# Performance work log

Hardware: AMD Instinct MI355X
Metric: run time of the kernel (lower is better)

The kernel has to match this reference:

```python
import jax, jax.numpy as jnp
import numpy as np

N_NODES = 50000
NEG_SLOPE = 0.2


def gat_layer(x, src, dst, W, a_src, a_dst, b, concat):
    # x: [N, Fin]; W: [Fin, H*C]; a_src/a_dst: [H, C]; b: [H*C] or [C]
    H, C = a_src.shape
    h = (x @ W).reshape(-1, H, C)                      # [N, H, C]
    al_s = jnp.einsum('nhc,hc->nh', h, a_src)          # [N, H]
    al_d = jnp.einsum('nhc,hc->nh', h, a_dst)          # [N, H]
    e = jax.nn.leaky_relu(al_s[src] + al_d[dst], NEG_SLOPE)   # [E, H]
    # segment softmax over incoming edges of each destination node
    e_max = jax.ops.segment_max(e, dst, num_segments=N_NODES)  # [N, H]
    ex = jnp.exp(e - e_max[dst])
    denom = jax.ops.segment_sum(ex, dst, num_segments=N_NODES)
    alpha = ex / (denom[dst] + 1e-16)                  # [E, H]
    msg = h[src] * alpha[:, :, None]                   # [E, H, C]
    out = jax.ops.segment_sum(msg, dst, num_segments=N_NODES)  # [N, H, C]
    out = out.reshape(N_NODES, H * C) if concat else out.mean(axis=1)
    return out + b


def setup_inputs() -> dict:
    key = jax.random.key(0)
    ks = jax.random.split(key, 16)
    x = jax.random.normal(ks[0], (N_NODES, 12), dtype=jnp.float32)
    edge_index = jax.random.randint(ks[1], (2, 400000), 0, N_NODES, dtype=jnp.int32)
    H, C = 8, 64
    s = 0.1
    W1 = jax.random.normal(ks[2], (12, H * C), jnp.float32) * s
    as1 = jax.random.normal(ks[3], (H, C), jnp.float32) * s
    ad1 = jax.random.normal(ks[4], (H, C), jnp.float32) * s
    b1 = jnp.zeros((H * C,), jnp.float32)
    W2 = jax.random.normal(ks[5], (H * C, H * C), jnp.float32) * s
    as2 = jax.random.normal(ks[6], (H, C), jnp.float32) * s
    ad2 = jax.random.normal(ks[7], (H, C), jnp.float32) * s
    b2 = jnp.zeros((H * C,), jnp.float32)
    W3 = jax.random.normal(ks[8], (H * C, H * 5), jnp.float32) * s
    as3 = jax.random.normal(ks[9], (H, 5), jnp.float32) * s
    ad3 = jax.random.normal(ks[10], (H, 5), jnp.float32) * s
    b3 = jnp.zeros((5,), jnp.float32)
    return {"x": x, "edge_index": edge_index,
            "W1": W1, "as1": as1, "ad1": ad1, "b1": b1,
            "W2": W2, "as2": as2, "ad2": ad2, "b2": b2,
            "W3": W3, "as3": as3, "ad3": ad3, "b3": b3}


def reference(x, edge_index, W1, as1, ad1, b1, W2, as2, ad2, b2, W3, as3, ad3, b3):
    # add self-loops (PyG GATConv default add_self_loops=True)
    loop = jnp.arange(N_NODES, dtype=edge_index.dtype)
    src = jnp.concatenate([edge_index[0], loop])
    dst = jnp.concatenate([edge_index[1], loop])
    h = gat_layer(x, src, dst, W1, as1, ad1, b1, concat=True)
    h = jax.nn.relu(h)
    h = gat_layer(h, src, dst, W2, as2, ad2, b2, concat=True)
    h = jax.nn.relu(h)
    h = gat_layer(h, src, dst, W3, as3, ad3, b3, concat=False)
    return jax.nn.log_softmax(h, axis=1)
```

## Files before the change

### kernel.cpp

```cpp
#include <hip/hip_runtime.h>
#include <hip/hip_bf16.h>

#define NN    50000
#define MP    50048
#define E0C   400000
#define ETOT  450000
#define HH    8
#define FF    512
#define F3    40
#define C3    5
#define MAXE  128
#define NBLK  ((NN + 1023) / 1024)
#define MT2   (MP / 128)
#define GT2   (MT2 * 4)

typedef __attribute__((ext_vector_type(8))) short bf16x8;
typedef __attribute__((ext_vector_type(8))) short s16x8;
typedef __attribute__((ext_vector_type(4))) float f32x4;

__device__ inline unsigned short f2bf(float f) {
    union { float f; unsigned int u; } v; v.f = f;
    unsigned int r = v.u + 0x7FFF + ((v.u >> 16) & 1);
    return (unsigned short)(r >> 16);
}
__device__ inline float bf2f(unsigned short u) {
    union { unsigned int i; float f; } v; v.i = ((unsigned int)u) << 16;
    return v.f;
}

__global__ void count_kernel(const int* __restrict__ ei, int* __restrict__ cnt) {
    int e = blockIdx.x * blockDim.x + threadIdx.x;
    if (e >= ETOT) return;
    int dst = (e < E0C) ? ei[E0C + e] : (e - E0C);
    atomicAdd(&cnt[dst], 1);
}

__global__ __launch_bounds__(1024) void scan_blocks(const int* __restrict__ cnt,
                                                    int* __restrict__ offs,
                                                    int* __restrict__ bsum) {
    __shared__ int s[1024];
    int tid = threadIdx.x;
    int i = blockIdx.x * 1024 + tid;
    s[tid] = (i < NN) ? cnt[i] : 0;
    __syncthreads();
    for (int d = 1; d < 1024; d <<= 1) {
        int add = (tid >= d) ? s[tid - d] : 0;
        __syncthreads();
        s[tid] += add;
        __syncthreads();
    }
    if (i < NN) offs[i + 1] = s[tid];
    if (tid == 1023) bsum[blockIdx.x] = s[1023];
}

__global__ __launch_bounds__(64) void scan_sums(int* __restrict__ bsum) {
    int lane = threadIdx.x;
    int v = (lane < NBLK) ? bsum[lane] : 0;
    int orig = v;
#pragma unroll
    for (int d = 1; d < 64; d <<= 1) {
        int o = __shfl_up(v, d);
        if (lane >= d) v += o;
    }
    if (lane < NBLK) bsum[lane] = v - orig;
}

__global__ __launch_bounds__(1024) void scan_add(int* __restrict__ offs,
                                                 const int* __restrict__ bsum) {
    int i = blockIdx.x * 1024 + threadIdx.x;
    if (i < NN) offs[i + 1] += bsum[blockIdx.x];
    if (i == 0) offs[0] = 0;
}

__global__ void scatter_kernel(const int* __restrict__ ei, const int* __restrict__ offs,
                               int* __restrict__ cur, int* __restrict__ srcs) {
    int e = blockIdx.x * blockDim.x + threadIdx.x;
    if (e >= ETOT) return;
    int src, dst;
    if (e < E0C) { src = ei[e]; dst = ei[E0C + e]; }
    else         { src = dst = e - E0C; }
    int pos = offs[dst] + atomicAdd(&cur[dst], 1);
    srcs[pos] = src;
}

__global__ __launch_bounds__(256) void gemm1_fused(
    const float* __restrict__ x, const float* __restrict__ W1,
    const float* __restrict__ as1, const float* __restrict__ ad1,
    unsigned short* __restrict__ hb, float* __restrict__ al_s,
    float* __restrict__ al_d) {
    __shared__ float xs[64 * 12];
    int t = threadIdx.x;
    int n0 = blockIdx.x * 64;
    int nvalid = NN - n0; if (nvalid > 64) nvalid = 64;

    for (int j = t; j < nvalid * 12; j += 256) xs[j] = x[(size_t)n0 * 12 + j];
    __syncthreads();

    int f = t * 2;
    float w0[12], w1[12];
#pragma unroll
    for (int k = 0; k < 12; ++k) {
        float2 wv = *(const float2*)&W1[k * FF + f];
        w0[k] = wv.x; w1[k] = wv.y;
    }
    float2 asv = *(const float2*)&as1[f];
    float2 adv = *(const float2*)&ad1[f];
    int head = t >> 5;

    for (int ni = 0; ni < nvalid; ++ni) {
        const float* xp = &xs[ni * 12];
        float4 xa = *(const float4*)xp;
        float4 xb = *(const float4*)(xp + 4);
        float4 xc = *(const float4*)(xp + 8);
        float xv[12] = {xa.x, xa.y, xa.z, xa.w, xb.x, xb.y, xb.z, xb.w,
                        xc.x, xc.y, xc.z, xc.w};
        float h0 = 0.f, h1 = 0.f;
#pragma unroll
        for (int k = 0; k < 12; ++k) { h0 += xv[k] * w0[k]; h1 += xv[k] * w1[k]; }
        unsigned int u = ((unsigned int)f2bf(h1) << 16) | f2bf(h0);
        *(unsigned int*)&hb[(size_t)(n0 + ni) * FF + f] = u;
        float ps = h0 * asv.x + h1 * asv.y;
        float pd = h0 * adv.x + h1 * adv.y;
#pragma unroll
        for (int d = 1; d < 32; d <<= 1) {
            ps += __shfl_xor(ps, d);
            pd += __shfl_xor(pd, d);
        }
        if ((t & 31) == 0) {
            al_s[(size_t)(n0 + ni) * HH + head] = ps;
            al_d[(size_t)(n0 + ni) * HH + head] = pd;
        }
    }
}

__global__ __launch_bounds__(256) void attn_gather(
    const unsigned short* __restrict__ Hb,
    const float* __restrict__ alS, const float* __restrict__ alD,
    const int* __restrict__ offs, const int* __restrict__ srcs,
    const float* __restrict__ bias,
    float* __restrict__ out_f32, unsigned short* __restrict__ out_b16, int relu) {
    __shared__ float alpha_sh[4][MAXE][HH];
    __shared__ int   srcs_sh[4][MAXE];
    int w = threadIdx.x >> 6, lane = threadIdx.x & 63;
    int n = blockIdx.x * 4 + w;
    if (n >= NN) return;
    int h = lane >> 3, es = lane & 7;
    int beg = offs[n], end = offs[n + 1], deg = end - beg;

    float ald = alD[n * HH + h];
    float m = -1e30f, den = 0.f, idn;

    if (deg <= MAXE) {
        for (int e = es; e < deg; e += 8) {
            int s = srcs[beg + e];
            if (h == 0) srcs_sh[w][e] = s;
            float sc = alS[s * HH + h] + ald;
            sc = sc > 0.f ? sc : 0.2f * sc;
            alpha_sh[w][e][h] = sc;
            m = fmaxf(m, sc);
        }
        m = fmaxf(m, __shfl_xor(m, 1));
        m = fmaxf(m, __shfl_xor(m, 2));
        m = fmaxf(m, __shfl_xor(m, 4));
        for (int e = es; e < deg; e += 8) {
            float ex = __expf(alpha_sh[w][e][h] - m);
            den += ex;
            alpha_sh[w][e][h] = ex;
        }
        den += __shfl_xor(den, 1);
        den += __shfl_xor(den, 2);
        den += __shfl_xor(den, 4);
        idn = 1.f / (den + 1e-16f);
    } else {
        for (int e = es; e < deg; e += 8) {
            int s = srcs[beg + e];
            float sc = alS[s * HH + h] + ald;
            sc = sc > 0.f ? sc : 0.2f * sc;
            m = fmaxf(m, sc);
        }
        m = fmaxf(m, __shfl_xor(m, 1));
        m = fmaxf(m, __shfl_xor(m, 2));
        m = fmaxf(m, __shfl_xor(m, 4));
        for (int e = es; e < deg; e += 8) {
            int s = srcs[beg + e];
            float sc = alS[s * HH + h] + ald;
            sc = sc > 0.f ? sc : 0.2f * sc;
            den += __expf(sc - m);
        }
        den += __shfl_xor(den, 1);
        den += __shfl_xor(den, 2);
        den += __shfl_xor(den, 4);
        idn = 1.f / (den + 1e-16f);
    }

    int f0 = lane * 8;
    float acc[8] = {};
    if (deg <= MAXE) {
        int e = 0;
        for (; e + 4 <= deg; e += 4) {
            int s0 = srcs_sh[w][e + 0], s1 = srcs_sh[w][e + 1];
            int s2 = srcs_sh[w][e + 2], s3 = srcs_sh[w][e + 3];
            bf16x8 v0 = *(const bf16x8*)&Hb[(size_t)s0 * FF + f0];
            bf16x8 v1 = *(const bf16x8*)&Hb[(size_t)s1 * FF + f0];
            bf16x8 v2 = *(const bf16x8*)&Hb[(size_t)s2 * FF + f0];
            bf16x8 v3 = *(const bf16x8*)&Hb[(size_t)s3 * FF + f0];
            float a0 = alpha_sh[w][e + 0][h], a1 = alpha_sh[w][e + 1][h];
            float a2 = alpha_sh[w][e + 2][h], a3 = alpha_sh[w][e + 3][h];
#pragma unroll
            for (int k = 0; k < 8; ++k) {
                acc[k] += a0 * bf2f((unsigned short)v0[k]);
                acc[k] += a1 * bf2f((unsigned short)v1[k]);
                acc[k] += a2 * bf2f((unsigned short)v2[k]);
                acc[k] += a3 * bf2f((unsigned short)v3[k]);
            }
        }
        for (; e < deg; ++e) {
            int s = srcs_sh[w][e];
            float a = alpha_sh[w][e][h];
            bf16x8 v = *(const bf16x8*)&Hb[(size_t)s * FF + f0];
#pragma unroll
            for (int k = 0; k < 8; ++k)
                acc[k] += a * bf2f((unsigned short)v[k]);
        }
#pragma unroll
        for (int k = 0; k < 8; ++k) acc[k] *= idn;
    } else {
        for (int e = 0; e < deg; ++e) {
            int s = srcs[beg + e];
            float sc = alS[s * HH + h] + ald;
            sc = sc > 0.f ? sc : 0.2f * sc;
            float a = __expf(sc - m) * idn;
            bf16x8 v = *(const bf16x8*)&Hb[(size_t)s * FF + f0];
#pragma unroll
            for (int k = 0; k < 8; ++k)
                acc[k] += a * bf2f((unsigned short)v[k]);
        }
    }
    float4 b0 = *(const float4*)&bias[f0];
    float4 b1 = *(const float4*)&bias[f0 + 4];
    float bv[8] = {b0.x, b0.y, b0.z, b0.w, b1.x, b1.y, b1.z, b1.w};
    float vv[8];
#pragma unroll
    for (int k = 0; k < 8; ++k) {
        float t = acc[k] + bv[k];
        vv[k] = relu ? fmaxf(t, 0.f) : t;
    }
    if (out_f32) {
        float4 o0 = {vv[0], vv[1], vv[2], vv[3]};
        float4 o1 = {vv[4], vv[5], vv[6], vv[7]};
        *(float4*)&out_f32[(size_t)n * FF + f0] = o0;
        *(float4*)&out_f32[(size_t)n * FF + f0 + 4] = o1;
    }
    if (out_b16) {
        s16x8 ov;
#pragma unroll
        for (int k = 0; k < 8; ++k) ov[k] = (short)f2bf(vv[k]);
        *(s16x8*)&out_b16[(size_t)n * FF + f0] = ov;
    }
}

__global__ void prep_w2t(const float* __restrict__ W2, unsigned short* __restrict__ W2T) {
    int i = blockIdx.x * blockDim.x + threadIdx.x;
    if (i >= FF * FF) return;
    int n = i >> 9, k = i & 511;
    W2T[i] = f2bf(W2[k * FF + n]);
}

__global__ void prep_w3t(const float* __restrict__ W3, unsigned short* __restrict__ W3T) {
    int i = blockIdx.x * blockDim.x + threadIdx.x;
    if (i >= 48 * 512) return;
    int n = i >> 9, k = i & 511;
    W3T[i] = (n < F3) ? f2bf(W3[k * F3 + n]) : 0;
}

__global__ __launch_bounds__(256) void gemm_mfma(
    const unsigned short* __restrict__ A,
    const unsigned short* __restrict__ BT,
    const float* __restrict__ a_s, const float* __restrict__ a_d,
    unsigned short* __restrict__ Cb,
    float* __restrict__ alS, float* __restrict__ alD,
    int N, int K) {
    __shared__ unsigned short As[2][128 * 64];
    __shared__ unsigned short Bs[2][128 * 64];
    int t = threadIdx.x;
    int wave = t >> 6, lane = t & 63;
    int wr = wave >> 1, wc = wave & 1;

    int bid = blockIdx.x;
    int mt, nt;
    if (bid < (MT2 / 8) * 32) {
        int g = bid >> 5, r = bid & 31;
        mt = g * 8 + (r & 7);
        nt = r >> 3;
    } else {
        int t2 = bid - (MT2 / 8) * 32;
        mt = (MT2 / 8) * 8 + (t2 >> 2);
        nt = t2 & 3;
    }
    int m0 = mt * 128, n0 = nt * 128;

    f32x4 acc[4][4] = {};
    int kg = lane >> 4;
    int lr = lane & 15;

    auto STAGE = [&](int buf, int k0) {
#pragma unroll
        for (int q = 0; q < 4; ++q) {
            int c   = q * 256 + t;
            int row = c >> 3, kc = c & 7;
            int kcs = kc ^ (row & 7);
            const unsigned short* ga = A + (size_t)(m0 + row) * K + k0 + kcs * 8;
            const unsigned short* gb = BT + (size_t)(n0 + row) * K + k0 + kcs * 8;
            unsigned short* la = &As[buf][(size_t)(q * 256 + wave * 64) * 8];
            unsigned short* lb = &Bs[buf][(size_t)(q * 256 + wave * 64) * 8];
            __builtin_amdgcn_global_load_lds(
                (const __attribute__((address_space(1))) void*)ga,
                (__attribute__((address_space(3))) void*)la, 16, 0, 0);
            __builtin_amdgcn_global_load_lds(
                (const __attribute__((address_space(1))) void*)gb,
                (__attribute__((address_space(3))) void*)lb, 16, 0, 0);
        }
    };

    const int NT = K / 64;
    STAGE(0, 0);
    __syncthreads();
    int cur = 0;
    for (int kt = 0; kt < NT; ++kt) {
        if (kt + 1 < NT) STAGE(cur ^ 1, (kt + 1) * 64);
        const unsigned short* Ac = As[cur];
        const unsigned short* Bc = Bs[cur];
#pragma unroll
        for (int ks = 0; ks < 2; ++ks) {
            bf16x8 af[4], bf[4];
#pragma unroll
            for (int i = 0; i < 4; ++i) {
                int rowa = wr * 64 + i * 16 + lr;
                af[i] = *(const bf16x8*)&Ac[rowa * 64 + (((ks << 2) | kg) ^ (rowa & 7)) * 8];
                int rowb = wc * 64 + i * 16 + lr;
                bf[i] = *(const bf16x8*)&Bc[rowb * 64 + (((ks << 2) | kg) ^ (rowb & 7)) * 8];
            }
#pragma unroll
            for (int i = 0; i < 4; ++i)
#pragma unroll
                for (int j = 0; j < 4; ++j)
                    acc[i][j] = __builtin_amdgcn_mfma_f32_16x16x32_bf16(
                        af[i], bf[j], acc[i][j], 0, 0, 0);
        }
        __syncthreads();
        cur ^= 1;
    }

    int head = (n0 >> 6) + wc;
    float asv[4], adv[4];
#pragma unroll
    for (int j = 0; j < 4; ++j) {
        int cc = n0 + wc * 64 + j * 16 + lr;
        asv[j] = a_s[cc];
        adv[j] = a_d[cc];
    }
#pragma unroll
    for (int i = 0; i < 4; ++i) {
#pragma unroll
        for (int reg = 0; reg < 4; ++reg) {
            float ps = 0.f, pd = 0.f;
#pragma unroll
            for (int j = 0; j < 4; ++j) {
                ps += acc[i][j][reg] * asv[j];
                pd += acc[i][j][reg] * adv[j];
            }
#pragma unroll
            for (int d = 1; d < 16; d <<= 1) {
                ps += __shfl_xor(ps, d);
                pd += __shfl_xor(pd, d);
            }
            if (lr == 0) {
                int r = m0 + wr * 64 + i * 16 + kg * 4 + reg;
                alS[(size_t)r * HH + head] = ps;
                alD[(size_t)r * HH + head] = pd;
            }
        }
    }

#pragma unroll
    for (int i = 0; i < 4; ++i) {
        int rb = m0 + wr * 64 + i * 16 + kg * 4;
#pragma unroll
        for (int j = 0; j < 4; ++j) {
            int cc = n0 + wc * 64 + j * 16 + lr;
#pragma unroll
            for (int reg = 0; reg < 4; ++reg)
                Cb[(size_t)(rb + reg) * N + cc] = f2bf(acc[i][j][reg]);
        }
    }
}

__global__ __launch_bounds__(256) void gemm3_mfma(
    const unsigned short* __restrict__ A,
    const unsigned short* __restrict__ BT,
    float* __restrict__ C) {
    __shared__ unsigned short As[128 * 64];
    __shared__ unsigned short Bs[48 * 64];
    int t = threadIdx.x;
    int wave = t >> 6, lane = t & 63;
    int m0 = blockIdx.x * 128;
    int kg = lane >> 4, lr = lane & 15;

    f32x4 acc[2][3] = {};

    for (int k0 = 0; k0 < 512; k0 += 64) {
#pragma unroll
        for (int q = 0; q < 4; ++q) {
            int c   = q * 256 + t;
            int row = c >> 3, kc = c & 7;
            int kcs = kc ^ (row & 7);
            const unsigned short* ga = A + (size_t)(m0 + row) * 512 + k0 + kcs * 8;
            unsigned short* la = &As[(size_t)(q * 256 + wave * 64) * 8];
            __builtin_amdgcn_global_load_lds(
                (const __attribute__((address_space(1))) void*)ga,
                (__attribute__((address_space(3))) void*)la, 16, 0, 0);
        }
        {
            int c   = t;
            int row = c >> 3, kc = c & 7;
            int kcs = kc ^ (row & 7);
            const unsigned short* gb = BT + (size_t)row * 512 + k0 + kcs * 8;
            unsigned short* lb = &Bs[(size_t)(wave * 64) * 8];
            __builtin_amdgcn_global_load_lds(
                (const __attribute__((address_space(1))) void*)gb,
                (__attribute__((address_space(3))) void*)lb, 16, 0, 0);
        }
        if (t < 128) {
            int c   = 256 + t;
            int row = c >> 3, kc = c & 7;
            int kcs = kc ^ (row & 7);
            const unsigned short* gb = BT + (size_t)row * 512 + k0 + kcs * 8;
            unsigned short* lb = &Bs[(size_t)(256 + wave * 64) * 8];
            __builtin_amdgcn_global_load_lds(
                (const __attribute__((address_space(1))) void*)gb,
                (__attribute__((address_space(3))) void*)lb, 16, 0, 0);
        }
        __syncthreads();
#pragma unroll
        for (int ks = 0; ks < 2; ++ks) {
            bf16x8 af[2], bf[3];
#pragma unroll
            for (int i = 0; i < 2; ++i) {
                int rowa = wave * 32 + i * 16 + lr;
                af[i] = *(const bf16x8*)&As[rowa * 64 + (((ks << 2) | kg) ^ (rowa & 7)) * 8];
            }
#pragma unroll
            for (int j = 0; j < 3; ++j) {
                int rowb = j * 16 + lr;
                bf[j] = *(const bf16x8*)&Bs[rowb * 64 + (((ks << 2) | kg) ^ (rowb & 7)) * 8];
            }
#pragma unroll
            for (int i = 0; i < 2; ++i)
#pragma unroll
                for (int j = 0; j < 3; ++j)
                    acc[i][j] = __builtin_amdgcn_mfma_f32_16x16x32_bf16(
                        af[i], bf[j], acc[i][j], 0, 0, 0);
        }
        __syncthreads();
    }

#pragma unroll
    for (int i = 0; i < 2; ++i) {
        int rb = m0 + wave * 32 + i * 16 + kg * 4;
#pragma unroll
        for (int j = 0; j < 3; ++j) {
            int cc = j * 16 + lr;
            if (cc >= F3) continue;
#pragma unroll
            for (int reg = 0; reg < 4; ++reg) {
                int r = rb + reg;
                if (r < NN) C[(size_t)r * F3 + cc] = acc[i][j][reg];
            }
        }
    }
}

__global__ void al40_kernel(const float* __restrict__ h3, const float* __restrict__ as3,
                            const float* __restrict__ ad3, float* __restrict__ al_s,
                            float* __restrict__ al_d) {
    int n = blockIdx.x * blockDim.x + threadIdx.x;
    if (n >= NN) return;
#pragma unroll
    for (int hh = 0; hh < HH; ++hh) {
        float s = 0.f, d = 0.f;
#pragma unroll
        for (int c = 0; c < C3; ++c) {
            float v = h3[(size_t)n * F3 + hh * C3 + c];
            s += v * as3[hh * C3 + c];
            d += v * ad3[hh * C3 + c];
        }
        al_s[n * HH + hh] = s;
        al_d[n * HH + hh] = d;
    }
}

__global__ __launch_bounds__(256) void attn3_kernel(
    const float* __restrict__ h3, const float* __restrict__ al_s,
    const float* __restrict__ al_d, const int* __restrict__ offs,
    const int* __restrict__ srcs, const float* __restrict__ b3,
    float* __restrict__ out) {
    __shared__ float alpha_sh[4][MAXE][HH];
    __shared__ int   srcs_sh[4][MAXE];
    __shared__ float idn_sh[4][HH], m_sh[4][HH], ald_sh2[4][HH];
    __shared__ float accs[4][F3];
    __shared__ float vv[4][C3];
    int w = threadIdx.x >> 6, lane = threadIdx.x & 63;
    int n = blockIdx.x * 4 + w;
    int h = lane >> 3, es = lane & 7;
    int beg = offs[n], end = offs[n + 1], deg = end - beg;

    float ald = al_d[n * HH + h];
    float m = -1e30f, den = 0.f, idn;
    if (deg <= MAXE) {
        for (int e = es; e < deg; e += 8) {
            int s = srcs[beg + e];
            if (h == 0) srcs_sh[w][e] = s;
            float sc = al_s[s * HH + h] + ald;
            sc = sc > 0.f ? sc : 0.2f * sc;
            alpha_sh[w][e][h] = sc;
            m = fmaxf(m, sc);
        }
        m = fmaxf(m, __shfl_xor(m, 1));
        m = fmaxf(m, __shfl_xor(m, 2));
        m = fmaxf(m, __shfl_xor(m, 4));
        for (int e = es; e < deg; e += 8) {
            float ex = __expf(alpha_sh[w][e][h] - m);
            den += ex;
            alpha_sh[w][e][h] = ex;
        }
        den += __shfl_xor(den, 1);
        den += __shfl_xor(den, 2);
        den += __shfl_xor(den, 4);
        idn = 1.f / (den + 1e-16f);
        if (es == 0) idn_sh[w][h] = idn;
    } else {
        for (int e = es; e < deg; e += 8) {
            int s = srcs[beg + e];
            float sc = al_s[s * HH + h] + ald;
            sc = sc > 0.f ? sc : 0.2f * sc;
            m = fmaxf(m, sc);
        }
        m = fmaxf(m, __shfl_xor(m, 1));
        m = fmaxf(m, __shfl_xor(m, 2));
        m = fmaxf(m, __shfl_xor(m, 4));
        for (int e = es; e < deg; e += 8) {
            int s = srcs[beg + e];
            float sc = al_s[s * HH + h] + ald;
            sc = sc > 0.f ? sc : 0.2f * sc;
            den += __expf(sc - m);
        }
        den += __shfl_xor(den, 1);
        den += __shfl_xor(den, 2);
        den += __shfl_xor(den, 4);
        idn = 1.f / (den + 1e-16f);
        if (es == 0) { idn_sh[w][h] = idn; m_sh[w][h] = m; ald_sh2[w][h] = ald; }
    }
    __syncthreads();

    if (lane < F3) {
        int hh = lane / C3;
        float acc = 0.f;
        if (deg <= MAXE) {
            int e = 0;
            for (; e + 4 <= deg; e += 4) {
                int s0 = srcs_sh[w][e + 0], s1 = srcs_sh[w][e + 1];
                int s2 = srcs_sh[w][e + 2], s3 = srcs_sh[w][e + 3];
                float v0 = h3[(size_t)s0 * F3 + lane];
                float v1 = h3[(size_t)s1 * F3 + lane];
                float v2 = h3[(size_t)s2 * F3 + lane];
                float v3 = h3[(size_t)s3 * F3 + lane];
                acc += alpha_sh[w][e + 0][hh] * v0 + alpha_sh[w][e + 1][hh] * v1
                     + alpha_sh[w][e + 2][hh] * v2 + alpha_sh[w][e + 3][hh] * v3;
            }
            for (; e < deg; ++e) {
                int s = srcs_sh[w][e];
                acc += alpha_sh[w][e][hh] * h3[(size_t)s * F3 + lane];
            }
        } else {
            float mm = m_sh[w][hh], aald = ald_sh2[w][hh];
            for (int e = 0; e < deg; ++e) {
                int s = srcs[beg + e];
                float sc = al_s[s * HH + hh] + aald;
                sc = sc > 0.f ? sc : 0.2f * sc;
                acc += __expf(sc - mm) * h3[(size_t)s * F3 + lane];
            }
        }
        accs[w][lane] = acc * idn_sh[w][hh];
    }
    __syncthreads();
    if (lane < C3) {
        float s = 0.f;
#pragma unroll
        for (int hh = 0; hh < HH; ++hh) s += accs[w][hh * C3 + lane];
        vv[w][lane] = s * 0.125f + b3[lane];
    }
    __syncthreads();
    if (lane < C3) {
        float mx = vv[w][0];
#pragma unroll
        for (int c = 1; c < C3; ++c) mx = fmaxf(mx, vv[w][c]);
        float se = 0.f;
#pragma unroll
        for (int c = 0; c < C3; ++c) se += __expf(vv[w][c] - mx);
        out[(size_t)n * C3 + lane] = vv[w][lane] - mx - logf(se);
    }
}

extern "C" void kernel_launch(void* const* d_in, const int* in_sizes, int n_in,
                              void* d_out, int out_size, void* d_ws, size_t ws_size,
                              hipStream_t stream) {
    const float* x   = (const float*)d_in[0];
    const int*   ei  = (const int*)d_in[1];
    const float* W1  = (const float*)d_in[2];
    const float* as1 = (const float*)d_in[3];
    const float* ad1 = (const float*)d_in[4];
    const float* b1  = (const float*)d_in[5];
    const float* W2  = (const float*)d_in[6];
    const float* as2 = (const float*)d_in[7];
    const float* ad2 = (const float*)d_in[8];
    const float* b2  = (const float*)d_in[9];
    const float* W3  = (const float*)d_in[10];
    const float* as3 = (const float*)d_in[11];
    const float* ad3 = (const float*)d_in[12];
    const float* b3  = (const float*)d_in[13];
    float* out = (float*)d_out;

    auto au = [](size_t v) { return (v + 255) & ~(size_t)255; };
    char* p = (char*)d_ws;
    size_t szHb = au((size_t)MP * FF * 2);
    char* r1 = p;
    unsigned short* Hb1 = (unsigned short*)r1;
    unsigned short* Hb2 = (unsigned short*)r1;
    p += szHb;
    char* r2 = p;
    unsigned short* A2   = (unsigned short*)r2;
    unsigned short* Bb16 = (unsigned short*)r2;
    unsigned short* W2T  = (unsigned short*)(r2 + szHb);
    p = r2 + szHb + au((size_t)FF * FF * 2);
    unsigned short* W3T = (unsigned short*)p;  p += au((size_t)48 * 512 * 2);
    float* alS  = (float*)p;  p += au((size_t)MP * HH * 4);
    float* alD  = (float*)p;  p += au((size_t)MP * HH * 4);
    float* h3   = (float*)p;  p += au((size_t)NN * F3 * 4);
    int* offs   = (int*)p;    p += au((size_t)(NN + 1) * 4);
    int* cnt    = (int*)p;    p += au((size_t)NN * 4);
    int* srcs   = (int*)p;    p += au((size_t)ETOT * 4);
    int* bsum   = (int*)p;    p += au(64 * 4);

    hipMemsetAsync(cnt, 0, (size_t)NN * 4, stream);
    count_kernel<<<(ETOT + 255) / 256, 256, 0, stream>>>(ei, cnt);
    scan_blocks<<<NBLK, 1024, 0, stream>>>(cnt, offs, bsum);
    scan_sums<<<1, 64, 0, stream>>>(bsum);
    scan_add<<<NBLK, 1024, 0, stream>>>(offs, bsum);
    hipMemsetAsync(cnt, 0, (size_t)NN * 4, stream);
    scatter_kernel<<<(ETOT + 255) / 256, 256, 0, stream>>>(ei, offs, cnt, srcs);
    hipMemsetAsync(A2 + (size_t)NN * FF, 0, (size_t)(MP - NN) * FF * 2, stream);
    prep_w2t<<<(FF * FF + 255) / 256, 256, 0, stream>>>(W2, W2T);
    prep_w3t<<<(48 * 512 + 255) / 256, 256, 0, stream>>>(W3, W3T);

    gemm1_fused<<<(NN + 63) / 64, 256, 0, stream>>>(x, W1, as1, ad1, Hb1, alS, alD);
    attn_gather<<<(NN + 3) / 4, 256, 0, stream>>>(Hb1, alS, alD, offs, srcs, b1,
                                                  nullptr, A2, 1);

    gemm_mfma<<<GT2, 256, 0, stream>>>(
        A2, W2T, as2, ad2, Hb2, alS, alD, FF, FF);
    attn_gather<<<(NN + 3) / 4, 256, 0, stream>>>(Hb2, alS, alD, offs, srcs, b2,
                                                  nullptr, Bb16, 1);

    gemm3_mfma<<<MP / 128, 256, 0, stream>>>(Bb16, W3T, h3);
    al40_kernel<<<(NN + 255) / 256, 256, 0, stream>>>(h3, as3, ad3, alS, alD);
    attn3_kernel<<<NN / 4, 256, 0, stream>>>(h3, alS, alD, offs, srcs, b3, out);
}
```

Before: 351.6 us.

## Fuse scan and prep launches; single-buffer LDS in layer-2 GEMM

Folds the block-sum scan into scan_add, so each block computes its own prefix with a wave reduction. Merges the W2/W3 transpose-convert kernels and the A2 padding memset into one prep kernel. Together these drop three launches from the pipeline. It also switches the layer-2 MFMA GEMM from double-buffered to single-buffered LDS, with a sync after each stage. That halves shared memory and may raise occupancy, but global loads no longer overlap with MFMA compute.

```diff
diff --git a/kernel.cpp b/kernel.cpp
--- a/kernel.cpp
+++ b/kernel.cpp
@@ -53,22 +53,19 @@
     if (tid == 1023) bsum[blockIdx.x] = s[1023];
 }
 
-__global__ __launch_bounds__(64) void scan_sums(int* __restrict__ bsum) {
-    int lane = threadIdx.x;
-    int v = (lane < NBLK) ? bsum[lane] : 0;
-    int orig = v;
-#pragma unroll
-    for (int d = 1; d < 64; d <<= 1) {
-        int o = __shfl_up(v, d);
-        if (lane >= d) v += o;
-    }
-    if (lane < NBLK) bsum[lane] = v - orig;
-}
-
 __global__ __launch_bounds__(1024) void scan_add(int* __restrict__ offs,
                                                  const int* __restrict__ bsum) {
-    int i = blockIdx.x * 1024 + threadIdx.x;
-    if (i < NN) offs[i + 1] += bsum[blockIdx.x];
+    __shared__ int pref;
+    int tid = threadIdx.x;
+    if (tid < 64) {
+        int v = (tid < blockIdx.x) ? bsum[tid] : 0;
+#pragma unroll
+        for (int d = 32; d; d >>= 1) v += __shfl_xor(v, d);
+        if (tid == 0) pref = v;
+    }
+    __syncthreads();
+    int i = blockIdx.x * 1024 + tid;
+    if (i < NN) offs[i + 1] += pref;
     if (i == 0) offs[0] = 0;
 }
 
@@ -81,6 +78,25 @@
     else         { src = dst = e - E0C; }
     int pos = offs[dst] + atomicAdd(&cur[dst], 1);
     srcs[pos] = src;
+}
+
+__global__ void prep_all(const float* __restrict__ W2, const float* __restrict__ W3,
+                         unsigned short* __restrict__ W2T, unsigned short* __restrict__ W3T,
+                         unsigned short* __restrict__ A2) {
+    int i = blockIdx.x * blockDim.x + threadIdx.x;
+    if (i < FF * FF) {
+        int n = i >> 9, k = i & 511;
+        W2T[i] = f2bf(W2[k * FF + n]);
+        return;
+    }
+    int j = i - FF * FF;
+    if (j < 48 * 512) {
+        int n = j >> 9, k = j & 511;
+        W3T[j] = (n < F3) ? f2bf(W3[k * F3 + n]) : 0;
+        return;
+    }
+    int l = j - 48 * 512;
+    if (l < (MP - NN) * FF) A2[(size_t)NN * FF + l] = 0;
 }
 
 __global__ __launch_bounds__(256) void gemm1_fused(
@@ -259,20 +275,6 @@
     }
 }
 
-__global__ void prep_w2t(const float* __restrict__ W2, unsigned short* __restrict__ W2T) {
-    int i = blockIdx.x * blockDim.x + threadIdx.x;
-    if (i >= FF * FF) return;
-    int n = i >> 9, k = i & 511;
-    W2T[i] = f2bf(W2[k * FF + n]);
-}
-
-__global__ void prep_w3t(const float* __restrict__ W3, unsigned short* __restrict__ W3T) {
-    int i = blockIdx.x * blockDim.x + threadIdx.x;
-    if (i >= 48 * 512) return;
-    int n = i >> 9, k = i & 511;
-    W3T[i] = (n < F3) ? f2bf(W3[k * F3 + n]) : 0;
-}
-
 __global__ __launch_bounds__(256) void gemm_mfma(
     const unsigned short* __restrict__ A,
     const unsigned short* __restrict__ BT,
@@ -280,8 +282,8 @@
     unsigned short* __restrict__ Cb,
     float* __restrict__ alS, float* __restrict__ alD,
     int N, int K) {
-    __shared__ unsigned short As[2][128 * 64];
-    __shared__ unsigned short Bs[2][128 * 64];
+    __shared__ unsigned short As[128 * 64];
+    __shared__ unsigned short Bs[128 * 64];
     int t = threadIdx.x;
     int wave = t >> 6, lane = t & 63;
     int wr = wave >> 1, wc = wave & 1;
@@ -303,7 +305,7 @@
     int kg = lane >> 4;
     int lr = lane & 15;
 
-    auto STAGE = [&](int buf, int k0) {
+    for (int k0 = 0; k0 < K; k0 += 64) {
 #pragma unroll
         for (int q = 0; q < 4; ++q) {
             int c   = q * 256 + t;
@@ -311,8 +313,8 @@
             int kcs = kc ^ (row & 7);
             const unsigned short* ga = A + (size_t)(m0 + row) * K + k0 + kcs * 8;
             const unsigned short* gb = BT + (size_t)(n0 + row) * K + k0 + kcs * 8;
-            unsigned short* la = &As[buf][(size_t)(q * 256 + wave * 64) * 8];
-            unsigned short* lb = &Bs[buf][(size_t)(q * 256 + wave * 64) * 8];
+            unsigned short* la = As + (size_t)(q * 256 + wave * 64) * 8;
+            unsigned short* lb = Bs + (size_t)(q * 256 + wave * 64) * 8;
             __builtin_amdgcn_global_load_lds(
                 (const __attribute__((address_space(1))) void*)ga,
                 (__attribute__((address_space(3))) void*)la, 16, 0, 0);
@@ -320,25 +322,16 @@
                 (const __attribute__((address_space(1))) void*)gb,
                 (__attribute__((address_space(3))) void*)lb, 16, 0, 0);
         }
-    };
-
-    const int NT = K / 64;
-    STAGE(0, 0);
-    __syncthreads();
-    int cur = 0;
-    for (int kt = 0; kt < NT; ++kt) {
-        if (kt + 1 < NT) STAGE(cur ^ 1, (kt + 1) * 64);
-        const unsigned short* Ac = As[cur];
-        const unsigned short* Bc = Bs[cur];
+        __syncthreads();
 #pragma unroll
         for (int ks = 0; ks < 2; ++ks) {
             bf16x8 af[4], bf[4];
 #pragma unroll
             for (int i = 0; i < 4; ++i) {
                 int rowa = wr * 64 + i * 16 + lr;
-                af[i] = *(const bf16x8*)&Ac[rowa * 64 + (((ks << 2) | kg) ^ (rowa & 7)) * 8];
+                af[i] = *(const bf16x8*)&As[rowa * 64 + (((ks << 2) | kg) ^ (rowa & 7)) * 8];
                 int rowb = wc * 64 + i * 16 + lr;
-                bf[i] = *(const bf16x8*)&Bc[rowb * 64 + (((ks << 2) | kg) ^ (rowb & 7)) * 8];
+                bf[i] = *(const bf16x8*)&Bs[rowb * 64 + (((ks << 2) | kg) ^ (rowb & 7)) * 8];
             }
 #pragma unroll
             for (int i = 0; i < 4; ++i)
@@ -348,7 +341,6 @@
                         af[i], bf[j], acc[i][j], 0, 0, 0);
         }
         __syncthreads();
-        cur ^= 1;
     }
 
     int head = (n0 >> 6) + wc;
@@ -654,13 +646,13 @@
     hipMemsetAsync(cnt, 0, (size_t)NN * 4, stream);
     count_kernel<<<(ETOT + 255) / 256, 256, 0, stream>>>(ei, cnt);
     scan_blocks<<<NBLK, 1024, 0, stream>>>(cnt, offs, bsum);
-    scan_sums<<<1, 64, 0, stream>>>(bsum);
     scan_add<<<NBLK, 1024, 0, stream>>>(offs, bsum);
     hipMemsetAsync(cnt, 0, (size_t)NN * 4, stream);
     scatter_kernel<<<(ETOT + 255) / 256, 256, 0, stream>>>(ei, offs, cnt, srcs);
-    hipMemsetAsync(A2 + (size_t)NN * FF, 0, (size_t)(MP - NN) * FF * 2, stream);
-    prep_w2t<<<(FF * FF + 255) / 256, 256, 0, stream>>>(W2, W2T);
-    prep_w3t<<<(48 * 512 + 255) / 256, 256, 0, stream>>>(W3, W3T);
+    {
+        int prep_elems = FF * FF + 48 * 512 + (MP - NN) * FF;
+        prep_all<<<(prep_elems + 255) / 256, 256, 0, stream>>>(W2, W3, W2T, W3T, A2);
+    }
 
     gemm1_fused<<<(NN + 63) / 64, 256, 0, stream>>>(x, W1, as1, ad1, Hb1, alS, alD);
     attn_gather<<<(NN + 3) / 4, 256, 0, stream>>>(Hb1, alS, alD, offs, srcs, b1,
```

Measured after the change: 356.5 us. About the same (+1.4%).
